# Kernel optimization log

Measured on AMD Instinct MI355X. Metric: run time of the kernel, lower is better.

Reference implementation:

```python
import jax, jax.numpy as jnp
import numpy as np
import math

B, S, D, H = 2, 2048, 1024, 16
DK = D // H


def setup_inputs() -> dict:
    key = jax.random.key(0)
    ks = jax.random.split(key, 12)
    scale = 1.0 / math.sqrt(D)
    inp = {
        "query": jax.random.normal(ks[0], (B, S, D), dtype=jnp.float32),
        "key": jax.random.normal(ks[1], (B, S, D), dtype=jnp.float32),
        "value": jax.random.normal(ks[2], (B, S, D), dtype=jnp.float32),
        # causal mask, broadcastable to [B, H, S, S]; 0 -> masked
        "mask": jnp.tril(jnp.ones((S, S), dtype=jnp.int32))[None, None],
        # linear params stored as [in, out] so y = x @ W + b
        "Wq": jax.random.normal(ks[3], (D, D), dtype=jnp.float32) * scale,
        "bq": jnp.zeros((D,), dtype=jnp.float32),
        "Wk": jax.random.normal(ks[4], (D, D), dtype=jnp.float32) * scale,
        "bk": jnp.zeros((D,), dtype=jnp.float32),
        "Wv": jax.random.normal(ks[5], (D, D), dtype=jnp.float32) * scale,
        "bv": jnp.zeros((D,), dtype=jnp.float32),
        "Wo": jax.random.normal(ks[6], (D, D), dtype=jnp.float32) * scale,
        "bo": jnp.zeros((D,), dtype=jnp.float32),
    }
    return inp


def reference(query, key, value, mask, Wq, bq, Wk, bk, Wv, bv, Wo, bo):
    b = query.shape[0]
    # QKV projections -> [b, H, S, DK]
    q = (query @ Wq + bq).reshape(b, -1, H, DK).transpose(0, 2, 1, 3)
    k = (key @ Wk + bk).reshape(b, -1, H, DK).transpose(0, 2, 1, 3)
    v = (value @ Wv + bv).reshape(b, -1, H, DK).transpose(0, 2, 1, 3)
    # scores [b, H, Sq, Sk]
    scores = jnp.einsum("bhqd,bhkd->bhqk", q, k) / math.sqrt(DK)
    scores = jnp.where(mask == 0, jnp.float32(-1e9), scores)
    attention_weights = jax.nn.softmax(scores, axis=-1)
    # dropout p=0.0 -> identity
    context = jnp.einsum("bhqk,bhkd->bhqd", attention_weights, v)
    context = context.transpose(0, 2, 1, 3).reshape(b, -1, H * DK)
    output = context @ Wo + bo
    return (output, attention_weights)
```

## Files before the change

### kernel.cpp

```cpp
#include <hip/hip_runtime.h>

typedef __bf16 bf16x8 __attribute__((ext_vector_type(8)));
typedef unsigned short u16x8 __attribute__((ext_vector_type(8)));
typedef unsigned short u16x4 __attribute__((ext_vector_type(4)));
typedef unsigned int u32x4 __attribute__((ext_vector_type(4)));
typedef float f32x4 __attribute__((ext_vector_type(4)));

#define MFMA16 __builtin_amdgcn_mfma_f32_16x16x32_bf16

static __device__ inline unsigned short f2bf(float f) {
    unsigned int u = __float_as_uint(f);
    u += 0x7fffu + ((u >> 16) & 1u);
    return (unsigned short)(u >> 16);
}
static __device__ inline unsigned int pack2(float a, float b) {
    return (unsigned int)f2bf(a) | ((unsigned int)f2bf(b) << 16);
}
static __device__ inline bf16x8 as_bf(u16x8 v) { return __builtin_bit_cast(bf16x8, v); }

static __device__ inline void gload_lds16(const unsigned short* g, unsigned short* l) {
    __builtin_amdgcn_global_load_lds(
        (const __attribute__((address_space(1))) void*)g,
        (__attribute__((address_space(3))) void*)l, 16, 0, 0);
}

__global__ __launch_bounds__(256) void conv3(
    const float* __restrict__ A0, const float* __restrict__ A1, const float* __restrict__ A2,
    unsigned short* __restrict__ O0, unsigned short* __restrict__ O1, unsigned short* __restrict__ O2)
{
    const float* A; unsigned short* O;
    switch (blockIdx.y) { case 0: A = A0; O = O0; break;
                          case 1: A = A1; O = O1; break;
                          default: A = A2; O = O2; break; }
    size_t i = ((size_t)blockIdx.x * 256 + threadIdx.x) * 8;
    float4 a = *(const float4*)(A + i);
    float4 b = *(const float4*)(A + i + 4);
    u16x8 o;
    o[0] = f2bf(a.x); o[1] = f2bf(a.y); o[2] = f2bf(a.z); o[3] = f2bf(a.w);
    o[4] = f2bf(b.x); o[5] = f2bf(b.y); o[6] = f2bf(b.z); o[7] = f2bf(b.w);
    *(u16x8*)(O + i) = o;
}

__global__ __launch_bounds__(256) void conv_wt(
    const float* __restrict__ W0, const float* __restrict__ W1,
    const float* __restrict__ W2, const float* __restrict__ W3,
    unsigned short* __restrict__ T0, unsigned short* __restrict__ T1,
    unsigned short* __restrict__ T2, unsigned short* __restrict__ T3)
{
    const float* W; unsigned short* T;
    switch (blockIdx.z) { case 0: W = W0; T = T0; break;
                          case 1: W = W1; T = T1; break;
                          case 2: W = W2; T = T2; break;
                          default: W = W3; T = T3; break; }
    __shared__ unsigned short L[64][72];
    int t = threadIdx.x;
    int r = t >> 2, cs = (t & 3) * 16;
    int r0 = blockIdx.y * 64, c0 = blockIdx.x * 64;
    const float* wp = W + (size_t)(r0 + r) * 1024 + c0 + cs;
    #pragma unroll
    for (int u = 0; u < 16; u += 4) {
        float4 f = *(const float4*)(wp + u);
        L[r][cs + u]     = f2bf(f.x);
        L[r][cs + u + 1] = f2bf(f.y);
        L[r][cs + u + 2] = f2bf(f.z);
        L[r][cs + u + 3] = f2bf(f.w);
    }
    __syncthreads();
    unsigned short* op = T + (size_t)(c0 + r) * 1024 + r0 + cs;
    u16x8 o0, o1;
    #pragma unroll
    for (int i2 = 0; i2 < 8; i2++) { o0[i2] = L[cs + i2][r]; o1[i2] = L[cs + 8 + i2][r]; }
    *(u16x8*)op = o0;
    *(u16x8*)(op + 8) = o1;
}

__global__ __launch_bounds__(256) void proj128(
    const unsigned short* __restrict__ Xq, const unsigned short* __restrict__ Xk,
    const unsigned short* __restrict__ Xv,
    const unsigned short* __restrict__ WqT, const unsigned short* __restrict__ WkT,
    const unsigned short* __restrict__ WvT,
    const float* __restrict__ bq, const float* __restrict__ bk, const float* __restrict__ bv,
    unsigned short* __restrict__ Qo, unsigned short* __restrict__ Ko,
    unsigned short* __restrict__ Vto)
{
    const unsigned short *X, *WT; const float* bias; float oscale;
    if (blockIdx.z == 0)      { X = Xq; WT = WqT; bias = bq; oscale = 0.125f; }
    else if (blockIdx.z == 1) { X = Xk; WT = WkT; bias = bk; oscale = 1.f; }
    else                      { X = Xv; WT = WvT; bias = bv; oscale = 1.f; }
    __shared__ __align__(16) unsigned short Al[128 * 32];
    __shared__ __align__(16) unsigned short Bl[128 * 32];
    const int tid = threadIdx.x, lane = tid & 63, wave = tid >> 6;
    const int li = lane & 15, lg = lane >> 4;
    const int wm = wave >> 1, wn = wave & 1;
    const int row0 = blockIdx.x * 128, n0 = blockIdx.y * 128;
    f32x4 acc[4][4] = {};
    const int srow = wave * 16 + (lane >> 2), sseg = lane & 3;
    const unsigned short* ga0 = X + (size_t)(row0 + srow) * 1024 + sseg * 8;
    const unsigned short* gb0 = WT + (size_t)(n0 + srow) * 1024 + sseg * 8;
    unsigned short* lA = &Al[wave * 512];
    unsigned short* lB = &Bl[wave * 512];
    for (int k0 = 0; k0 < 1024; k0 += 32) {
        gload_lds16(ga0 + k0, lA);
        gload_lds16(ga0 + 64 * 1024 + k0, lA + 2048);
        gload_lds16(gb0 + k0, lB);
        gload_lds16(gb0 + 64 * 1024 + k0, lB + 2048);
        __syncthreads();
        bf16x8 af[4], bfr[4];
        #pragma unroll
        for (int i = 0; i < 4; i++)
            af[i] = as_bf(*(const u16x8*)&Al[(wm * 64 + i * 16 + li) * 32 + lg * 8]);
        #pragma unroll
        for (int j = 0; j < 4; j++)
            bfr[j] = as_bf(*(const u16x8*)&Bl[(wn * 64 + j * 16 + li) * 32 + lg * 8]);
        #pragma unroll
        for (int i = 0; i < 4; i++)
            #pragma unroll
            for (int j = 0; j < 4; j++)
                acc[i][j] = MFMA16(af[i], bfr[j], acc[i][j], 0, 0, 0);
        __syncthreads();
    }
    const int b = row0 >> 11;
    if (blockIdx.z == 2) {
        #pragma unroll
        for (int j = 0; j < 4; j++) {
            int n = n0 + wn * 64 + j * 16 + li;
            float bb = bias[n];
            int h = n >> 6, dk = n & 63;
            unsigned short* ob = Vto + ((size_t)(b * 16 + h) * 64 + dk) * 2048;
            #pragma unroll
            for (int i = 0; i < 4; i++) {
                int s = (row0 + wm * 64 + i * 16 + lg * 4) & 2047;
                u16x4 pk;
                pk[0] = f2bf(acc[i][j][0] + bb);
                pk[1] = f2bf(acc[i][j][1] + bb);
                pk[2] = f2bf(acc[i][j][2] + bb);
                pk[3] = f2bf(acc[i][j][3] + bb);
                *(u16x4*)(ob + s) = pk;
            }
        }
    } else {
        unsigned short* out = (blockIdx.z == 0) ? Qo : Ko;
        #pragma unroll
        for (int j = 0; j < 4; j++) {
            int n = n0 + wn * 64 + j * 16 + li;
            float bb = bias[n];
            int h = n >> 6, dk = n & 63;
            unsigned short* ob = out + ((size_t)(b * 16 + h) * 2048) * 64 + dk;
            #pragma unroll
            for (int i = 0; i < 4; i++)
                #pragma unroll
                for (int r = 0; r < 4; r++) {
                    int s = (row0 + wm * 64 + i * 16 + lg * 4 + r) & 2047;
                    ob[(size_t)s * 64] = f2bf((acc[i][j][r] + bb) * oscale);
                }
        }
    }
}

__global__ __launch_bounds__(256) void final128(
    const unsigned short* __restrict__ A, const unsigned short* __restrict__ WT,
    const float* __restrict__ bias, float* __restrict__ out)
{
    __shared__ __align__(16) unsigned short Al[128 * 32];
    __shared__ __align__(16) unsigned short Bl[128 * 32];
    const int tid = threadIdx.x, lane = tid & 63, wave = tid >> 6;
    const int li = lane & 15, lg = lane >> 4;
    const int wm = wave >> 1, wn = wave & 1;
    const int row0 = blockIdx.x * 128, n0 = blockIdx.y * 128;
    f32x4 acc[4][4] = {};
    const int srow = wave * 16 + (lane >> 2), sseg = lane & 3;
    const unsigned short* ga0 = A + (size_t)(row0 + srow) * 1024 + sseg * 8;
    const unsigned short* gb0 = WT + (size_t)(n0 + srow) * 1024 + sseg * 8;
    unsigned short* lA = &Al[wave * 512];
    unsigned short* lB = &Bl[wave * 512];
    for (int k0 = 0; k0 < 1024; k0 += 32) {
        gload_lds16(ga0 + k0, lA);
        gload_lds16(ga0 + 64 * 1024 + k0, lA + 2048);
        gload_lds16(gb0 + k0, lB);
        gload_lds16(gb0 + 64 * 1024 + k0, lB + 2048);
        __syncthreads();
        bf16x8 af[4], bfr[4];
        #pragma unroll
        for (int i = 0; i < 4; i++)
            af[i] = as_bf(*(const u16x8*)&Al[(wm * 64 + i * 16 + li) * 32 + lg * 8]);
        #pragma unroll
        for (int j = 0; j < 4; j++)
            bfr[j] = as_bf(*(const u16x8*)&Bl[(wn * 64 + j * 16 + li) * 32 + lg * 8]);
        #pragma unroll
        for (int i = 0; i < 4; i++)
            #pragma unroll
            for (int j = 0; j < 4; j++)
                acc[i][j] = MFMA16(af[i], bfr[j], acc[i][j], 0, 0, 0);
        __syncthreads();
    }
    #pragma unroll
    for (int j = 0; j < 4; j++) {
        int n = n0 + wn * 64 + j * 16 + li;
        float bb = bias[n];
        #pragma unroll
        for (int i = 0; i < 4; i++)
            #pragma unroll
            for (int r = 0; r < 4; r++) {
                int row = row0 + wm * 64 + i * 16 + lg * 4 + r;
                out[(size_t)row * 1024 + n] = acc[i][j][r] + bb;
            }
    }
}

__global__ __launch_bounds__(256, 4) void attn_fused(
    const unsigned short* __restrict__ Q, const unsigned short* __restrict__ K,
    const unsigned short* __restrict__ Vt,
    float* __restrict__ wOut, unsigned short* __restrict__ ctx)
{
    __shared__ __align__(16) unsigned short Kl[2][4096];
    __shared__ __align__(16) unsigned short Vl[2][4096];
    const int tid = threadIdx.x, lane = tid & 63, wave = tid >> 6;
    const int li = lane & 15, lg = lane >> 4;
    const int y = blockIdx.y;
    const int bh = blockIdx.x * 4 + (y >> 4);
    const int t = y & 15;
    const int b = bh >> 4, h = bh & 15;
    const unsigned short* Kb = K + (size_t)bh * 2048 * 64;
    const unsigned short* Vb = Vt + (size_t)bh * 64 * 2048;
    const int aSel = 32 * (lg & 1);
    const bool hiT = lg >= 2;

    auto stageK = [&](int u, int buf) {
        const unsigned short* base = Kb + (size_t)u * 64 * 64;
        #pragma unroll
        for (int c = 0; c < 2; c++) {
            int s16 = c * 256 + wave * 64 + lane;
            int row = s16 >> 3, uu = s16 & 7;
            int ul = uu ^ (row & 7);
            gload_lds16(base + row * 64 + ul * 8,
                        &Kl[buf][(size_t)(c * 256 + wave * 64) * 8]);
        }
    };
    auto stageV = [&](int u, int buf) {
        #pragma unroll
        for (int c = 0; c < 2; c++) {
            int s16 = c * 256 + wave * 64 + lane;
            int row = s16 >> 3, uu = s16 & 7;
            int ul = uu ^ (row & 7);
            gload_lds16(Vb + (size_t)row * 2048 + u * 64 + ul * 8,
                        &Vl[buf][(size_t)(c * 256 + wave * 64) * 8]);
        }
    };
    auto kfrag = [&](const unsigned short* KB, int tt, int hf) -> bf16x8 {
        int row = tt * 16 + li;
        int st = ((hf * 4 + lg) ^ (li & 7));
        return as_bf(*(const u16x8*)&KB[row * 64 + st * 8]);
    };
    auto vfrag = [&](const unsigned short* VB, int g, int c2l) -> bf16x8 {
        int row = g * 16 + li;
        int st = ((c2l * 4 + lg) ^ (li & 7));
        return as_bf(*(const u16x8*)&VB[row * 64 + st * 8]);
    };

    #pragma unroll 1
    for (int pass = 0; pass < 2; ++pass) {
        const int Mt = pass ? (31 - t) : t;
        const int q0 = Mt * 64;
        const int M16 = Mt * 4 + wave;
        const int nun = Mt + 1;
        const unsigned short* Qp = Q + ((size_t)bh * 2048 + q0 + wave * 16 + li) * 64 + lg * 8;
        bf16x8 qa0 = as_bf(*(const u16x8*)Qp);
        bf16x8 qa1 = as_bf(*(const u16x8*)(Qp + 32));

        float lsum = 0.f;
        stageK(0, 0);
        __syncthreads();
        #pragma unroll 1
        for (int u = 0; u < nun; ++u) {
            if (u + 1 < nun) stageK(u + 1, (u + 1) & 1);
            const unsigned short* KB = &Kl[u & 1][0];
            #pragma unroll
            for (int tt = 0; tt < 4; tt++) {
                int kts = u * 4 + tt;
                if (kts <= M16) {
                    f32x4 s = {0.f, 0.f, 0.f, 0.f};
                    s = MFMA16(kfrag(KB, tt, 0), qa0, s, 0, 0, 0);
                    s = MFMA16(kfrag(KB, tt, 1), qa1, s, 0, 0, 0);
                    if (kts < M16) {
                        lsum += __expf(s[0]) + __expf(s[1]) + __expf(s[2]) + __expf(s[3]);
                    } else {
                        #pragma unroll
                        for (int r = 0; r < 4; r++)
                            if (lg * 4 + r <= li) lsum += __expf(s[r]);
                    }
                }
            }
            __syncthreads();
        }
        lsum += __shfl_xor(lsum, 16);
        lsum += __shfl_xor(lsum, 32);
        const float rinv = 1.f / lsum;

        stageK(0, 0);
        stageV(0, 0);
        __syncthreads();
        float* wRow = wOut + (size_t)bh * 2048 * 2048 + (size_t)(q0 + wave * 16 + li) * 2048;
        f32x4 o0 = {}, o1 = {}, o2 = {}, o3 = {};
        #pragma unroll 1
        for (int u = 0; u < nun; ++u) {
            if (u + 1 < nun) { stageK(u + 1, (u + 1) & 1); stageV(u + 1, (u + 1) & 1); }
            const unsigned short* KB = &Kl[u & 1][0];
            const unsigned short* VB = &Vl[u & 1][0];
            #pragma unroll
            for (int c2l = 0; c2l < 2; c2l++) {
                unsigned pk0, pk1, pk2, pk3;
                #pragma unroll
                for (int st = 0; st < 2; st++) {
                    int kts = u * 4 + c2l * 2 + st;
                    f32x4 w = {0.f, 0.f, 0.f, 0.f};
                    if (kts <= M16) {
                        f32x4 s = {0.f, 0.f, 0.f, 0.f};
                        int tt = c2l * 2 + st;
                        s = MFMA16(kfrag(KB, tt, 0), qa0, s, 0, 0, 0);
                        s = MFMA16(kfrag(KB, tt, 1), qa1, s, 0, 0, 0);
                        bool diag = (kts == M16);
                        #pragma unroll
                        for (int r = 0; r < 4; r++) {
                            float pv = __expf(s[r]);
                            if (diag && (lg * 4 + r) > li) pv = 0.f;
                            w[r] = pv * rinv;
                        }
                    }
                    *(f32x4*)(wRow + kts * 16 + lg * 4) = w;
                    if (st == 0) { pk0 = pack2(w[0], w[1]); pk1 = pack2(w[2], w[3]); }
                    else         { pk2 = pack2(w[0], w[1]); pk3 = pack2(w[2], w[3]); }
                }
                if (u * 4 + c2l * 2 <= M16) {
                    int srcA = li + aSel, srcB = srcA + 16;
                    unsigned ga0v = __shfl(pk0, srcA), ga1v = __shfl(pk1, srcA);
                    unsigned ga2v = __shfl(pk2, srcA), ga3v = __shfl(pk3, srcA);
                    unsigned gb0v = __shfl(pk0, srcB), gb1v = __shfl(pk1, srcB);
                    unsigned gb2v = __shfl(pk2, srcB), gb3v = __shfl(pk3, srcB);
                    u32x4 fr;
                    fr[0] = hiT ? ga2v : ga0v;
                    fr[1] = hiT ? ga3v : ga1v;
                    fr[2] = hiT ? gb2v : gb0v;
                    fr[3] = hiT ? gb3v : gb1v;
                    bf16x8 pa = __builtin_bit_cast(bf16x8, fr);
                    o0 = MFMA16(pa, vfrag(VB, 0, c2l), o0, 0, 0, 0);
                    o1 = MFMA16(pa, vfrag(VB, 1, c2l), o1, 0, 0, 0);
                    o2 = MFMA16(pa, vfrag(VB, 2, c2l), o2, 0, 0, 0);
                    o3 = MFMA16(pa, vfrag(VB, 3, c2l), o3, 0, 0, 0);
                }
            }
            __syncthreads();
        }
        {
            int kcov = nun * 64;
            f32x4 z = {0.f, 0.f, 0.f, 0.f};
            for (int c = kcov + lg * 4; c < 2048; c += 16)
                *(f32x4*)(wRow + c) = z;
        }
        #pragma unroll
        for (int r = 0; r < 4; r++) {
            int row = q0 + wave * 16 + lg * 4 + r;
            unsigned short* cp = ctx + (((size_t)(b * 2048 + row)) * 16 + h) * 64 + li;
            cp[0]  = f2bf(o0[r]);
            cp[16] = f2bf(o1[r]);
            cp[32] = f2bf(o2[r]);
            cp[48] = f2bf(o3[r]);
        }
    }
}

extern "C" void kernel_launch(void* const* d_in, const int* in_sizes, int n_in,
                              void* d_out, int out_size, void* d_ws, size_t ws_size,
                              hipStream_t stream) {
    const float* q_in = (const float*)d_in[0];
    const float* k_in = (const float*)d_in[1];
    const float* v_in = (const float*)d_in[2];
    const float* Wq = (const float*)d_in[4];
    const float* bq = (const float*)d_in[5];
    const float* Wk = (const float*)d_in[6];
    const float* bk = (const float*)d_in[7];
    const float* Wv = (const float*)d_in[8];
    const float* bv = (const float*)d_in[9];
    const float* Wo = (const float*)d_in[10];
    const float* bo = (const float*)d_in[11];

    float* out = (float*)d_out;
    float* wOut = out + 4194304;

    unsigned short* ws16 = (unsigned short*)d_ws;
    unsigned short* Xqb = ws16;
    unsigned short* Xkb = ws16 + 4194304;
    unsigned short* Xvb = ws16 + 8388608;
    unsigned short* WqT = ws16 + 12582912;
    unsigned short* WkT = WqT + 1048576;
    unsigned short* WvT = WkT + 1048576;
    unsigned short* WoT = WvT + 1048576;
    unsigned short* Qws = ws16 + 16777216;
    unsigned short* Kws = Qws + 4194304;
    unsigned short* Vtws = Kws + 4194304;
    unsigned short* ctxp = Vtws + 4194304;

    conv3<<<dim3(2048, 3), 256, 0, stream>>>(q_in, k_in, v_in, Xqb, Xkb, Xvb);
    conv_wt<<<dim3(16, 16, 4), 256, 0, stream>>>(Wq, Wk, Wv, Wo, WqT, WkT, WvT, WoT);
    proj128<<<dim3(32, 8, 3), 256, 0, stream>>>(Xqb, Xkb, Xvb, WqT, WkT, WvT,
                                                bq, bk, bv, Qws, Kws, Vtws);
    attn_fused<<<dim3(8, 64), 256, 0, stream>>>(Qws, Kws, Vtws, wOut, ctxp);
    final128<<<dim3(32, 8), 256, 0, stream>>>(ctxp, WoT, bo, out);
}
```

Baseline: 301.0 us.

## Process paired causal query tiles jointly, sharing K/V staging and staging P through LDS

The attention kernel used to run two sequential passes, one for query tile t and one for 31-t, each restaging K and V. Now both tiles are handled in a single loop, so each staged K/V tile and its V fragments feed both. The probability tiles go through a swizzled LDS buffer, and whole 64-column row segments are then written to global memory with coalesced stores in place of the scattered 16-byte stores. Tile ordering is interleaved across blocks and occupancy is lowered to 2 blocks per CU to fit the extra LDS and registers, which risks less latency hiding.

Result: faster. 270.8 us (-10.0%).

```diff
diff --git a/kernel.cpp b/kernel.cpp
--- a/kernel.cpp
+++ b/kernel.cpp
@@ -207,21 +207,29 @@
     }
 }
 
-__global__ __launch_bounds__(256, 4) void attn_fused(
+__global__ __launch_bounds__(256, 2) void attn_fused(
     const unsigned short* __restrict__ Q, const unsigned short* __restrict__ K,
     const unsigned short* __restrict__ Vt,
     float* __restrict__ wOut, unsigned short* __restrict__ ctx)
 {
     __shared__ __align__(16) unsigned short Kl[2][4096];
     __shared__ __align__(16) unsigned short Vl[2][4096];
+    __shared__ __align__(16) float PstA[4][16 * 64];
+    __shared__ __align__(16) float PstB[4][16 * 64];
     const int tid = threadIdx.x, lane = tid & 63, wave = tid >> 6;
     const int li = lane & 15, lg = lane >> 4;
     const int y = blockIdx.y;
     const int bh = blockIdx.x * 4 + (y >> 4);
-    const int t = y & 15;
+    const int g = y & 15;
+    const int t = (g & 1) ? (g >> 1) : (15 - (g >> 1));
+    const int tA = t, tB = 31 - t;
+    const int q0A = tA * 64, q0B = tB * 64;
+    const int M16A = tA * 4 + wave, M16B = tB * 4 + wave;
+    const int nunA = tA + 1, nunB = tB + 1;
     const int b = bh >> 4, h = bh & 15;
     const unsigned short* Kb = K + (size_t)bh * 2048 * 64;
     const unsigned short* Vb = Vt + (size_t)bh * 64 * 2048;
+    float* wHead = wOut + (size_t)bh * 2048 * 2048;
     const int aSel = 32 * (lg & 1);
     const bool hiT = lg >= 2;
 
@@ -251,120 +259,204 @@
         int st = ((hf * 4 + lg) ^ (li & 7));
         return as_bf(*(const u16x8*)&KB[row * 64 + st * 8]);
     };
-    auto vfrag = [&](const unsigned short* VB, int g, int c2l) -> bf16x8 {
-        int row = g * 16 + li;
+    auto vfrag = [&](const unsigned short* VB, int gg, int c2l) -> bf16x8 {
+        int row = gg * 16 + li;
         int st = ((c2l * 4 + lg) ^ (li & 7));
         return as_bf(*(const u16x8*)&VB[row * 64 + st * 8]);
     };
-
+    auto storePst = [&](const float* P, int q0t, int u) {
+        #pragma unroll
+        for (int i = 0; i < 4; ++i) {
+            int row = (lane >> 4) + i * 4;
+            int slot = lane & 15;
+            f32x4 val = *(const f32x4*)&P[row * 64 + ((slot ^ (row & 7)) * 4)];
+            *(f32x4*)(wHead + (size_t)(q0t + wave * 16 + row) * 2048 + u * 64 + slot * 4) = val;
+        }
+    };
+
+    const unsigned short* QpA = Q + ((size_t)bh * 2048 + q0A + wave * 16 + li) * 64 + lg * 8;
+    const unsigned short* QpB = Q + ((size_t)bh * 2048 + q0B + wave * 16 + li) * 64 + lg * 8;
+    bf16x8 qaA0 = as_bf(*(const u16x8*)QpA);
+    bf16x8 qaA1 = as_bf(*(const u16x8*)(QpA + 32));
+    bf16x8 qaB0 = as_bf(*(const u16x8*)QpB);
+    bf16x8 qaB1 = as_bf(*(const u16x8*)(QpB + 32));
+
+    float lsumA = 0.f, lsumB = 0.f;
+    stageK(0, 0);
+    __syncthreads();
     #pragma unroll 1
-    for (int pass = 0; pass < 2; ++pass) {
-        const int Mt = pass ? (31 - t) : t;
-        const int q0 = Mt * 64;
-        const int M16 = Mt * 4 + wave;
-        const int nun = Mt + 1;
-        const unsigned short* Qp = Q + ((size_t)bh * 2048 + q0 + wave * 16 + li) * 64 + lg * 8;
-        bf16x8 qa0 = as_bf(*(const u16x8*)Qp);
-        bf16x8 qa1 = as_bf(*(const u16x8*)(Qp + 32));
-
-        float lsum = 0.f;
-        stageK(0, 0);
+    for (int u = 0; u < nunB; ++u) {
+        if (u + 1 < nunB) stageK(u + 1, (u + 1) & 1);
+        const unsigned short* KB = &Kl[u & 1][0];
+        #pragma unroll
+        for (int tt = 0; tt < 4; tt++) {
+            int kts = u * 4 + tt;
+            if (kts <= M16B) {
+                f32x4 s = {0.f, 0.f, 0.f, 0.f};
+                s = MFMA16(kfrag(KB, tt, 0), qaB0, s, 0, 0, 0);
+                s = MFMA16(kfrag(KB, tt, 1), qaB1, s, 0, 0, 0);
+                if (kts < M16B) {
+                    lsumB += __expf(s[0]) + __expf(s[1]) + __expf(s[2]) + __expf(s[3]);
+                } else {
+                    #pragma unroll
+                    for (int r = 0; r < 4; r++)
+                        if (lg * 4 + r <= li) lsumB += __expf(s[r]);
+                }
+            }
+            if (kts <= M16A) {
+                f32x4 s = {0.f, 0.f, 0.f, 0.f};
+                s = MFMA16(kfrag(KB, tt, 0), qaA0, s, 0, 0, 0);
+                s = MFMA16(kfrag(KB, tt, 1), qaA1, s, 0, 0, 0);
+                if (kts < M16A) {
+                    lsumA += __expf(s[0]) + __expf(s[1]) + __expf(s[2]) + __expf(s[3]);
+                } else {
+                    #pragma unroll
+                    for (int r = 0; r < 4; r++)
+                        if (lg * 4 + r <= li) lsumA += __expf(s[r]);
+                }
+            }
+        }
         __syncthreads();
-        #pragma unroll 1
-        for (int u = 0; u < nun; ++u) {
-            if (u + 1 < nun) stageK(u + 1, (u + 1) & 1);
-            const unsigned short* KB = &Kl[u & 1][0];
-            #pragma unroll
-            for (int tt = 0; tt < 4; tt++) {
-                int kts = u * 4 + tt;
-                if (kts <= M16) {
-                    f32x4 s = {0.f, 0.f, 0.f, 0.f};
-                    s = MFMA16(kfrag(KB, tt, 0), qa0, s, 0, 0, 0);
-                    s = MFMA16(kfrag(KB, tt, 1), qa1, s, 0, 0, 0);
-                    if (kts < M16) {
-                        lsum += __expf(s[0]) + __expf(s[1]) + __expf(s[2]) + __expf(s[3]);
-                    } else {
-                        #pragma unroll
-                        for (int r = 0; r < 4; r++)
-                            if (lg * 4 + r <= li) lsum += __expf(s[r]);
-                    }
-                }
-            }
-            __syncthreads();
-        }
-        lsum += __shfl_xor(lsum, 16);
-        lsum += __shfl_xor(lsum, 32);
-        const float rinv = 1.f / lsum;
-
-        stageK(0, 0);
-        stageV(0, 0);
-        __syncthreads();
-        float* wRow = wOut + (size_t)bh * 2048 * 2048 + (size_t)(q0 + wave * 16 + li) * 2048;
-        f32x4 o0 = {}, o1 = {}, o2 = {}, o3 = {};
-        #pragma unroll 1
-        for (int u = 0; u < nun; ++u) {
-            if (u + 1 < nun) { stageK(u + 1, (u + 1) & 1); stageV(u + 1, (u + 1) & 1); }
-            const unsigned short* KB = &Kl[u & 1][0];
-            const unsigned short* VB = &Vl[u & 1][0];
-            #pragma unroll
-            for (int c2l = 0; c2l < 2; c2l++) {
+    }
+    lsumA += __shfl_xor(lsumA, 16); lsumA += __shfl_xor(lsumA, 32);
+    lsumB += __shfl_xor(lsumB, 16); lsumB += __shfl_xor(lsumB, 32);
+    const float rinvA = 1.f / lsumA;
+    const float rinvB = 1.f / lsumB;
+
+    stageK(0, 0);
+    stageV(0, 0);
+    __syncthreads();
+    f32x4 oA0 = {}, oA1 = {}, oA2 = {}, oA3 = {};
+    f32x4 oB0 = {}, oB1 = {}, oB2 = {}, oB3 = {};
+    float* PA = &PstA[wave][0];
+    float* PB = &PstB[wave][0];
+    #pragma unroll 1
+    for (int u = 0; u < nunB; ++u) {
+        if (u + 1 < nunB) { stageK(u + 1, (u + 1) & 1); stageV(u + 1, (u + 1) & 1); }
+        const unsigned short* KB = &Kl[u & 1][0];
+        const unsigned short* VB = &Vl[u & 1][0];
+        const bool liveA = (u < nunA);
+        #pragma unroll
+        for (int c2l = 0; c2l < 2; c2l++) {
+            bf16x8 vb0 = vfrag(VB, 0, c2l), vb1 = vfrag(VB, 1, c2l);
+            bf16x8 vb2 = vfrag(VB, 2, c2l), vb3 = vfrag(VB, 3, c2l);
+            {
                 unsigned pk0, pk1, pk2, pk3;
                 #pragma unroll
                 for (int st = 0; st < 2; st++) {
-                    int kts = u * 4 + c2l * 2 + st;
+                    int tt = c2l * 2 + st, kts = u * 4 + tt;
                     f32x4 w = {0.f, 0.f, 0.f, 0.f};
-                    if (kts <= M16) {
+                    if (kts <= M16B) {
                         f32x4 s = {0.f, 0.f, 0.f, 0.f};
-                        int tt = c2l * 2 + st;
-                        s = MFMA16(kfrag(KB, tt, 0), qa0, s, 0, 0, 0);
-                        s = MFMA16(kfrag(KB, tt, 1), qa1, s, 0, 0, 0);
-                        bool diag = (kts == M16);
+                        s = MFMA16(kfrag(KB, tt, 0), qaB0, s, 0, 0, 0);
+                        s = MFMA16(kfrag(KB, tt, 1), qaB1, s, 0, 0, 0);
+                        bool diag = (kts == M16B);
                         #pragma unroll
                         for (int r = 0; r < 4; r++) {
                             float pv = __expf(s[r]);
                             if (diag && (lg * 4 + r) > li) pv = 0.f;
-                            w[r] = pv * rinv;
+                            w[r] = pv * rinvB;
                         }
                     }
-                    *(f32x4*)(wRow + kts * 16 + lg * 4) = w;
+                    *(f32x4*)&PB[li * 64 + ((tt * 4 + lg) ^ (li & 7)) * 4] = w;
                     if (st == 0) { pk0 = pack2(w[0], w[1]); pk1 = pack2(w[2], w[3]); }
                     else         { pk2 = pack2(w[0], w[1]); pk3 = pack2(w[2], w[3]); }
                 }
-                if (u * 4 + c2l * 2 <= M16) {
-                    int srcA = li + aSel, srcB = srcA + 16;
+                if (u * 4 + c2l * 2 <= M16B) {
+                    int srcA = li + aSel, srcB2 = srcA + 16;
                     unsigned ga0v = __shfl(pk0, srcA), ga1v = __shfl(pk1, srcA);
                     unsigned ga2v = __shfl(pk2, srcA), ga3v = __shfl(pk3, srcA);
-                    unsigned gb0v = __shfl(pk0, srcB), gb1v = __shfl(pk1, srcB);
-                    unsigned gb2v = __shfl(pk2, srcB), gb3v = __shfl(pk3, srcB);
+                    unsigned gb0v = __shfl(pk0, srcB2), gb1v = __shfl(pk1, srcB2);
+                    unsigned gb2v = __shfl(pk2, srcB2), gb3v = __shfl(pk3, srcB2);
                     u32x4 fr;
                     fr[0] = hiT ? ga2v : ga0v;
                     fr[1] = hiT ? ga3v : ga1v;
                     fr[2] = hiT ? gb2v : gb0v;
                     fr[3] = hiT ? gb3v : gb1v;
                     bf16x8 pa = __builtin_bit_cast(bf16x8, fr);
-                    o0 = MFMA16(pa, vfrag(VB, 0, c2l), o0, 0, 0, 0);
-                    o1 = MFMA16(pa, vfrag(VB, 1, c2l), o1, 0, 0, 0);
-                    o2 = MFMA16(pa, vfrag(VB, 2, c2l), o2, 0, 0, 0);
-                    o3 = MFMA16(pa, vfrag(VB, 3, c2l), o3, 0, 0, 0);
-                }
-            }
-            __syncthreads();
-        }
-        {
-            int kcov = nun * 64;
-            f32x4 z = {0.f, 0.f, 0.f, 0.f};
-            for (int c = kcov + lg * 4; c < 2048; c += 16)
-                *(f32x4*)(wRow + c) = z;
-        }
-        #pragma unroll
-        for (int r = 0; r < 4; r++) {
-            int row = q0 + wave * 16 + lg * 4 + r;
-            unsigned short* cp = ctx + (((size_t)(b * 2048 + row)) * 16 + h) * 64 + li;
-            cp[0]  = f2bf(o0[r]);
-            cp[16] = f2bf(o1[r]);
-            cp[32] = f2bf(o2[r]);
-            cp[48] = f2bf(o3[r]);
-        }
+                    oB0 = MFMA16(pa, vb0, oB0, 0, 0, 0);
+                    oB1 = MFMA16(pa, vb1, oB1, 0, 0, 0);
+                    oB2 = MFMA16(pa, vb2, oB2, 0, 0, 0);
+                    oB3 = MFMA16(pa, vb3, oB3, 0, 0, 0);
+                }
+            }
+            if (liveA) {
+                unsigned pk0, pk1, pk2, pk3;
+                #pragma unroll
+                for (int st = 0; st < 2; st++) {
+                    int tt = c2l * 2 + st, kts = u * 4 + tt;
+                    f32x4 w = {0.f, 0.f, 0.f, 0.f};
+                    if (kts <= M16A) {
+                        f32x4 s = {0.f, 0.f, 0.f, 0.f};
+                        s = MFMA16(kfrag(KB, tt, 0), qaA0, s, 0, 0, 0);
+                        s = MFMA16(kfrag(KB, tt, 1), qaA1, s, 0, 0, 0);
+                        bool diag = (kts == M16A);
+                        #pragma unroll
+                        for (int r = 0; r < 4; r++) {
+                            float pv = __expf(s[r]);
+                            if (diag && (lg * 4 + r) > li) pv = 0.f;
+                            w[r] = pv * rinvA;
+                        }
+                    }
+                    *(f32x4*)&PA[li * 64 + ((tt * 4 + lg) ^ (li & 7)) * 4] = w;
+                    if (st == 0) { pk0 = pack2(w[0], w[1]); pk1 = pack2(w[2], w[3]); }
+                    else         { pk2 = pack2(w[0], w[1]); pk3 = pack2(w[2], w[3]); }
+                }
+                if (u * 4 + c2l * 2 <= M16A) {
+                    int srcA = li + aSel, srcB2 = srcA + 16;
+                    unsigned ga0v = __shfl(pk0, srcA), ga1v = __shfl(pk1, srcA);
+                    unsigned ga2v = __shfl(pk2, srcA), ga3v = __shfl(pk3, srcA);
+                    unsigned gb0v = __shfl(pk0, srcB2), gb1v = __shfl(pk1, srcB2);
+                    unsigned gb2v = __shfl(pk2, srcB2), gb3v = __shfl(pk3, srcB2);
+                    u32x4 fr;
+                    fr[0] = hiT ? ga2v : ga0v;
+                    fr[1] = hiT ? ga3v : ga1v;
+                    fr[2] = hiT ? gb2v : gb0v;
+                    fr[3] = hiT ? gb3v : gb1v;
+                    bf16x8 pa = __builtin_bit_cast(bf16x8, fr);
+                    oA0 = MFMA16(pa, vb0, oA0, 0, 0, 0);
+                    oA1 = MFMA16(pa, vb1, oA1, 0, 0, 0);
+                    oA2 = MFMA16(pa, vb2, oA2, 0, 0, 0);
+                    oA3 = MFMA16(pa, vb3, oA3, 0, 0, 0);
+                }
+            }
+        }
+        __builtin_amdgcn_s_waitcnt(0xC07F);
+        storePst(PB, q0B, u);
+        if (liveA) storePst(PA, q0A, u);
+        __syncthreads();
+    }
+    {
+        f32x4 z = {0.f, 0.f, 0.f, 0.f};
+        const int kcovA = nunA * 64, kcovB = nunB * 64;
+        #pragma unroll 1
+        for (int rr = 0; rr < 16; ++rr) {
+            float* bpA = wHead + (size_t)(q0A + wave * 16 + rr) * 2048;
+            for (int cb = kcovA; cb < 2048; cb += 256) {
+                int c = cb + lane * 4;
+                if (c < 2048) *(f32x4*)(bpA + c) = z;
+            }
+            float* bpB = wHead + (size_t)(q0B + wave * 16 + rr) * 2048;
+            for (int cb = kcovB; cb < 2048; cb += 256) {
+                int c = cb + lane * 4;
+                if (c < 2048) *(f32x4*)(bpB + c) = z;
+            }
+        }
+    }
+    #pragma unroll
+    for (int r = 0; r < 4; r++) {
+        int rowA = q0A + wave * 16 + lg * 4 + r;
+        unsigned short* cpA = ctx + (((size_t)(b * 2048 + rowA)) * 16 + h) * 64 + li;
+        cpA[0]  = f2bf(oA0[r]);
+        cpA[16] = f2bf(oA1[r]);
+        cpA[32] = f2bf(oA2[r]);
+        cpA[48] = f2bf(oA3[r]);
+        int rowB = q0B + wave * 16 + lg * 4 + r;
+        unsigned short* cpB = ctx + (((size_t)(b * 2048 + rowB)) * 16 + h) * 64 + li;
+        cpB[0]  = f2bf(oB0[r]);
+        cpB[16] = f2bf(oB1[r]);
+        cpB[32] = f2bf(oB2[r]);
+        cpB[48] = f2bf(oB3[r]);
     }
 }
 
```

## Stage attention weights in LDS for coalesced row stores and use 512-thread blocks

Applied to the files above, without the earlier changes.

The attention kernel now runs 8 waves per block, each block covering 128 query rows. The old two-pass pairing of light and heavy causal tiles is replaced by an index mapping that balances load across blocks. Each wave writes its softmax probabilities to a swizzled LDS tile and then re-reads them row-wise, so the global stores of the attention-weight matrix become full 256-byte contiguous rows instead of scattered 16-byte pieces. The upper-triangle zero fill is also rewritten to store whole rows per lane. This adds 32KB of LDS per block, which may reduce occupancy, and adds extra LDS traffic.

Measured after the change: 266.8 us. -11.4%, faster.

```diff
diff --git a/kernel.cpp b/kernel.cpp
--- a/kernel.cpp
+++ b/kernel.cpp
@@ -207,44 +207,41 @@
     }
 }
 
-__global__ __launch_bounds__(256, 4) void attn_fused(
+__global__ __launch_bounds__(512, 4) void attn_fused(
     const unsigned short* __restrict__ Q, const unsigned short* __restrict__ K,
     const unsigned short* __restrict__ Vt,
     float* __restrict__ wOut, unsigned short* __restrict__ ctx)
 {
     __shared__ __align__(16) unsigned short Kl[2][4096];
     __shared__ __align__(16) unsigned short Vl[2][4096];
+    __shared__ __align__(16) float PstW[8][16 * 64];
     const int tid = threadIdx.x, lane = tid & 63, wave = tid >> 6;
     const int li = lane & 15, lg = lane >> 4;
     const int y = blockIdx.y;
-    const int bh = blockIdx.x * 4 + (y >> 4);
-    const int t = y & 15;
+    const int bh = blockIdx.x * 4 + (y & 3);
+    const int p = y >> 2;
+    const int T = (p < 8) ? p : 23 - p;
     const int b = bh >> 4, h = bh & 15;
+    const int q0 = T * 128;
+    const int M16 = T * 8 + wave;
+    const int nunB = T * 2 + 2;
     const unsigned short* Kb = K + (size_t)bh * 2048 * 64;
     const unsigned short* Vb = Vt + (size_t)bh * 64 * 2048;
+    float* wHead = wOut + (size_t)bh * 2048 * 2048;
     const int aSel = 32 * (lg & 1);
     const bool hiT = lg >= 2;
 
     auto stageK = [&](int u, int buf) {
-        const unsigned short* base = Kb + (size_t)u * 64 * 64;
-        #pragma unroll
-        for (int c = 0; c < 2; c++) {
-            int s16 = c * 256 + wave * 64 + lane;
-            int row = s16 >> 3, uu = s16 & 7;
-            int ul = uu ^ (row & 7);
-            gload_lds16(base + row * 64 + ul * 8,
-                        &Kl[buf][(size_t)(c * 256 + wave * 64) * 8]);
-        }
+        int row = tid >> 3, uu = tid & 7;
+        int ul = uu ^ (row & 7);
+        gload_lds16(Kb + (size_t)u * 4096 + row * 64 + ul * 8,
+                    &Kl[buf][(size_t)tid * 8]);
     };
     auto stageV = [&](int u, int buf) {
-        #pragma unroll
-        for (int c = 0; c < 2; c++) {
-            int s16 = c * 256 + wave * 64 + lane;
-            int row = s16 >> 3, uu = s16 & 7;
-            int ul = uu ^ (row & 7);
-            gload_lds16(Vb + (size_t)row * 2048 + u * 64 + ul * 8,
-                        &Vl[buf][(size_t)(c * 256 + wave * 64) * 8]);
-        }
+        int row = tid >> 3, uu = tid & 7;
+        int ul = uu ^ (row & 7);
+        gload_lds16(Vb + (size_t)row * 2048 + u * 64 + ul * 8,
+                    &Vl[buf][(size_t)tid * 8]);
     };
     auto kfrag = [&](const unsigned short* KB, int tt, int hf) -> bf16x8 {
         int row = tt * 16 + li;
@@ -257,114 +254,121 @@
         return as_bf(*(const u16x8*)&VB[row * 64 + st * 8]);
     };
 
+    const unsigned short* Qp = Q + ((size_t)bh * 2048 + q0 + wave * 16 + li) * 64 + lg * 8;
+    bf16x8 qa0 = as_bf(*(const u16x8*)Qp);
+    bf16x8 qa1 = as_bf(*(const u16x8*)(Qp + 32));
+
+    float lsum = 0.f;
+    stageK(0, 0);
+    __syncthreads();
     #pragma unroll 1
-    for (int pass = 0; pass < 2; ++pass) {
-        const int Mt = pass ? (31 - t) : t;
-        const int q0 = Mt * 64;
-        const int M16 = Mt * 4 + wave;
-        const int nun = Mt + 1;
-        const unsigned short* Qp = Q + ((size_t)bh * 2048 + q0 + wave * 16 + li) * 64 + lg * 8;
-        bf16x8 qa0 = as_bf(*(const u16x8*)Qp);
-        bf16x8 qa1 = as_bf(*(const u16x8*)(Qp + 32));
-
-        float lsum = 0.f;
-        stageK(0, 0);
-        __syncthreads();
-        #pragma unroll 1
-        for (int u = 0; u < nun; ++u) {
-            if (u + 1 < nun) stageK(u + 1, (u + 1) & 1);
-            const unsigned short* KB = &Kl[u & 1][0];
-            #pragma unroll
-            for (int tt = 0; tt < 4; tt++) {
+    for (int u = 0; u < nunB; ++u) {
+        if (u + 1 < nunB) stageK(u + 1, (u + 1) & 1);
+        const unsigned short* KB = &Kl[u & 1][0];
+        #pragma unroll
+        for (int tt = 0; tt < 4; tt++) {
+            int kts = u * 4 + tt;
+            if (kts <= M16) {
+                f32x4 s = {0.f, 0.f, 0.f, 0.f};
+                s = MFMA16(kfrag(KB, tt, 0), qa0, s, 0, 0, 0);
+                s = MFMA16(kfrag(KB, tt, 1), qa1, s, 0, 0, 0);
+                if (kts < M16) {
+                    lsum += __expf(s[0]) + __expf(s[1]) + __expf(s[2]) + __expf(s[3]);
+                } else {
+                    #pragma unroll
+                    for (int r = 0; r < 4; r++)
+                        if (lg * 4 + r <= li) lsum += __expf(s[r]);
+                }
+            }
+        }
+        __syncthreads();
+    }
+    lsum += __shfl_xor(lsum, 16);
+    lsum += __shfl_xor(lsum, 32);
+    const float rinv = 1.f / lsum;
+
+    stageK(0, 0);
+    stageV(0, 0);
+    __syncthreads();
+    f32x4 o0 = {}, o1 = {}, o2 = {}, o3 = {};
+    float* Pw = &PstW[wave][0];
+    #pragma unroll 1
+    for (int u = 0; u < nunB; ++u) {
+        if (u + 1 < nunB) { stageK(u + 1, (u + 1) & 1); stageV(u + 1, (u + 1) & 1); }
+        const unsigned short* KB = &Kl[u & 1][0];
+        const unsigned short* VB = &Vl[u & 1][0];
+        #pragma unroll
+        for (int c2l = 0; c2l < 2; c2l++) {
+            unsigned pk0, pk1, pk2, pk3;
+            #pragma unroll
+            for (int st = 0; st < 2; st++) {
+                int tt = c2l * 2 + st;
                 int kts = u * 4 + tt;
+                f32x4 w = {0.f, 0.f, 0.f, 0.f};
                 if (kts <= M16) {
                     f32x4 s = {0.f, 0.f, 0.f, 0.f};
                     s = MFMA16(kfrag(KB, tt, 0), qa0, s, 0, 0, 0);
                     s = MFMA16(kfrag(KB, tt, 1), qa1, s, 0, 0, 0);
-                    if (kts < M16) {
-                        lsum += __expf(s[0]) + __expf(s[1]) + __expf(s[2]) + __expf(s[3]);
-                    } else {
-                        #pragma unroll
-                        for (int r = 0; r < 4; r++)
-                            if (lg * 4 + r <= li) lsum += __expf(s[r]);
+                    bool diag = (kts == M16);
+                    #pragma unroll
+                    for (int r = 0; r < 4; r++) {
+                        float pv = __expf(s[r]);
+                        if (diag && (lg * 4 + r) > li) pv = 0.f;
+                        w[r] = pv * rinv;
                     }
                 }
-            }
-            __syncthreads();
-        }
-        lsum += __shfl_xor(lsum, 16);
-        lsum += __shfl_xor(lsum, 32);
-        const float rinv = 1.f / lsum;
-
-        stageK(0, 0);
-        stageV(0, 0);
-        __syncthreads();
-        float* wRow = wOut + (size_t)bh * 2048 * 2048 + (size_t)(q0 + wave * 16 + li) * 2048;
-        f32x4 o0 = {}, o1 = {}, o2 = {}, o3 = {};
+                *(f32x4*)&Pw[li * 64 + ((tt * 4 + lg) ^ (li & 7)) * 4] = w;
+                if (st == 0) { pk0 = pack2(w[0], w[1]); pk1 = pack2(w[2], w[3]); }
+                else         { pk2 = pack2(w[0], w[1]); pk3 = pack2(w[2], w[3]); }
+            }
+            if (u * 4 + c2l * 2 <= M16) {
+                int srcA = li + aSel, srcB = srcA + 16;
+                unsigned ga0v = __shfl(pk0, srcA), ga1v = __shfl(pk1, srcA);
+                unsigned ga2v = __shfl(pk2, srcA), ga3v = __shfl(pk3, srcA);
+                unsigned gb0v = __shfl(pk0, srcB), gb1v = __shfl(pk1, srcB);
+                unsigned gb2v = __shfl(pk2, srcB), gb3v = __shfl(pk3, srcB);
+                u32x4 fr;
+                fr[0] = hiT ? ga2v : ga0v;
+                fr[1] = hiT ? ga3v : ga1v;
+                fr[2] = hiT ? gb2v : gb0v;
+                fr[3] = hiT ? gb3v : gb1v;
+                bf16x8 pa = __builtin_bit_cast(bf16x8, fr);
+                o0 = MFMA16(pa, vfrag(VB, 0, c2l), o0, 0, 0, 0);
+                o1 = MFMA16(pa, vfrag(VB, 1, c2l), o1, 0, 0, 0);
+                o2 = MFMA16(pa, vfrag(VB, 2, c2l), o2, 0, 0, 0);
+                o3 = MFMA16(pa, vfrag(VB, 3, c2l), o3, 0, 0, 0);
+            }
+        }
+        __builtin_amdgcn_s_waitcnt(0xC07F);
+        #pragma unroll
+        for (int i = 0; i < 4; ++i) {
+            int row = i * 4 + (lane >> 4);
+            int slot = lane & 15;
+            f32x4 val = *(const f32x4*)&Pw[row * 64 + ((slot ^ (row & 7)) * 4)];
+            *(f32x4*)(wHead + (size_t)(q0 + wave * 16 + row) * 2048 + u * 64 + slot * 4) = val;
+        }
+        __syncthreads();
+    }
+    {
+        const int kcov = nunB * 64;
+        f32x4 z = {0.f, 0.f, 0.f, 0.f};
         #pragma unroll 1
-        for (int u = 0; u < nun; ++u) {
-            if (u + 1 < nun) { stageK(u + 1, (u + 1) & 1); stageV(u + 1, (u + 1) & 1); }
-            const unsigned short* KB = &Kl[u & 1][0];
-            const unsigned short* VB = &Vl[u & 1][0];
-            #pragma unroll
-            for (int c2l = 0; c2l < 2; c2l++) {
-                unsigned pk0, pk1, pk2, pk3;
-                #pragma unroll
-                for (int st = 0; st < 2; st++) {
-                    int kts = u * 4 + c2l * 2 + st;
-                    f32x4 w = {0.f, 0.f, 0.f, 0.f};
-                    if (kts <= M16) {
-                        f32x4 s = {0.f, 0.f, 0.f, 0.f};
-                        int tt = c2l * 2 + st;
-                        s = MFMA16(kfrag(KB, tt, 0), qa0, s, 0, 0, 0);
-                        s = MFMA16(kfrag(KB, tt, 1), qa1, s, 0, 0, 0);
-                        bool diag = (kts == M16);
-                        #pragma unroll
-                        for (int r = 0; r < 4; r++) {
-                            float pv = __expf(s[r]);
-                            if (diag && (lg * 4 + r) > li) pv = 0.f;
-                            w[r] = pv * rinv;
-                        }
-                    }
-                    *(f32x4*)(wRow + kts * 16 + lg * 4) = w;
-                    if (st == 0) { pk0 = pack2(w[0], w[1]); pk1 = pack2(w[2], w[3]); }
-                    else         { pk2 = pack2(w[0], w[1]); pk3 = pack2(w[2], w[3]); }
-                }
-                if (u * 4 + c2l * 2 <= M16) {
-                    int srcA = li + aSel, srcB = srcA + 16;
-                    unsigned ga0v = __shfl(pk0, srcA), ga1v = __shfl(pk1, srcA);
-                    unsigned ga2v = __shfl(pk2, srcA), ga3v = __shfl(pk3, srcA);
-                    unsigned gb0v = __shfl(pk0, srcB), gb1v = __shfl(pk1, srcB);
-                    unsigned gb2v = __shfl(pk2, srcB), gb3v = __shfl(pk3, srcB);
-                    u32x4 fr;
-                    fr[0] = hiT ? ga2v : ga0v;
-                    fr[1] = hiT ? ga3v : ga1v;
-                    fr[2] = hiT ? gb2v : gb0v;
-                    fr[3] = hiT ? gb3v : gb1v;
-                    bf16x8 pa = __builtin_bit_cast(bf16x8, fr);
-                    o0 = MFMA16(pa, vfrag(VB, 0, c2l), o0, 0, 0, 0);
-                    o1 = MFMA16(pa, vfrag(VB, 1, c2l), o1, 0, 0, 0);
-                    o2 = MFMA16(pa, vfrag(VB, 2, c2l), o2, 0, 0, 0);
-                    o3 = MFMA16(pa, vfrag(VB, 3, c2l), o3, 0, 0, 0);
-                }
-            }
-            __syncthreads();
-        }
-        {
-            int kcov = nun * 64;
-            f32x4 z = {0.f, 0.f, 0.f, 0.f};
-            for (int c = kcov + lg * 4; c < 2048; c += 16)
-                *(f32x4*)(wRow + c) = z;
-        }
-        #pragma unroll
-        for (int r = 0; r < 4; r++) {
-            int row = q0 + wave * 16 + lg * 4 + r;
-            unsigned short* cp = ctx + (((size_t)(b * 2048 + row)) * 16 + h) * 64 + li;
-            cp[0]  = f2bf(o0[r]);
-            cp[16] = f2bf(o1[r]);
-            cp[32] = f2bf(o2[r]);
-            cp[48] = f2bf(o3[r]);
-        }
+        for (int rr = 0; rr < 16; ++rr) {
+            float* bp = wHead + (size_t)(q0 + wave * 16 + rr) * 2048;
+            for (int cb = kcov; cb < 2048; cb += 256) {
+                int c = cb + lane * 4;
+                if (c < 2048) *(f32x4*)(bp + c) = z;
+            }
+        }
+    }
+    #pragma unroll
+    for (int r = 0; r < 4; r++) {
+        int row = q0 + wave * 16 + lg * 4 + r;
+        unsigned short* cp = ctx + (((size_t)(b * 2048 + row)) * 16 + h) * 64 + li;
+        cp[0]  = f2bf(o0[r]);
+        cp[16] = f2bf(o1[r]);
+        cp[32] = f2bf(o2[r]);
+        cp[48] = f2bf(o3[r]);
     }
 }
 
@@ -403,6 +407,6 @@
     conv_wt<<<dim3(16, 16, 4), 256, 0, stream>>>(Wq, Wk, Wv, Wo, WqT, WkT, WvT, WoT);
     proj128<<<dim3(32, 8, 3), 256, 0, stream>>>(Xqb, Xkb, Xvb, WqT, WkT, WvT,
                                                 bq, bk, bv, Qws, Kws, Vtws);
-    attn_fused<<<dim3(8, 64), 256, 0, stream>>>(Qws, Kws, Vtws, wOut, ctxp);
+    attn_fused<<<dim3(8, 64), 512, 0, stream>>>(Qws, Kws, Vtws, wOut, ctxp);
     final128<<<dim3(32, 8), 256, 0, stream>>>(ctxp, WoT, bo, out);
 }
```
